# Kernel tuning notes

Measured on AMD Instinct MI355X. Metric: run time of the kernel, lower is better.

The kernel has to match this reference:

```python
import jax, jax.numpy as jnp
import numpy as np

NUM_CLASSES = 3
WINDOW = 5.0        # window_size for local connectivity
NUM_ITERS = 5       # mean-field iterations
THETA_BETA = 1.0    # smoothness kernel weight
TEMP = 1.0          # softmax temperature
H, W = 96, 96
B = 1


def setup_inputs() -> dict:
    key = jax.random.key(0)
    unary = jax.random.normal(key, (B, NUM_CLASSES, H, W), dtype=jnp.float32)
    # nn.Parameter(torch.eye(num_classes))
    compatibility = jnp.eye(NUM_CLASSES, dtype=jnp.float32)
    return {"unary": unary, "compatibility": compatibility}


def _pairwise_kernel(h, w):
    """Dense smoothness * local-connectivity kernel [N, N], N = h*w."""
    yy, xx = jnp.meshgrid(jnp.arange(h, dtype=jnp.float32),
                          jnp.arange(w, dtype=jnp.float32), indexing='ij')
    coords = jnp.stack([yy.ravel(), xx.ravel()], axis=-1)          # [N, 2]
    diff = coords[:, None, :] - coords[None, :, :]                 # [N, N, 2]
    dist = jnp.sqrt(jnp.sum(diff * diff, axis=-1))                 # cdist, [N, N]
    n = h * w
    conn = (dist <= WINDOW).astype(jnp.float32)
    conn = conn.at[jnp.arange(n), jnp.arange(n)].set(0.0)          # fill_diagonal_(0)
    smooth = jnp.exp(-THETA_BETA * dist)
    return smooth * conn                                           # [N, N]


def reference(unary, compatibility):
    b, c, h, w = unary.shape
    n = h * w
    unary_flat = unary.reshape(b, c, n)                            # [B, C, N]
    q = jax.nn.softmax(unary_flat / TEMP, axis=1)
    pairwise = _pairwise_kernel(h, w)                              # [N, N] (features=None path)
    for _ in range(NUM_ITERS):
        # messages[b,c,n] = sum_m pairwise[n,m] * q[b,c,m]  (bmm + transpose)
        messages = jnp.einsum('nm,bcm->bcn', pairwise, q)
        comp_msg = jnp.einsum('cd,bdn->bcn', compatibility, messages)
        q = jax.nn.softmax((unary_flat + comp_msg) / TEMP, axis=1)
    return q.reshape(b, c, h, w)
```

## Files before the change

kernel.cpp:

```cpp
#include <hip/hip_runtime.h>


constexpr int HH = 96, WW = 96, NN = HH * WW;
constexpr int T = 8, HALO = 5, EXT = T + 2 * HALO;

template <bool FIRST, bool LAST>
__global__ __launch_bounds__(64) void crf_iter(
    const float* __restrict__ unary,
    const float* __restrict__ comp,
    const float4* __restrict__ qin,
    float4* __restrict__ qnext,
    float* __restrict__ qout)
{
    __shared__ float4 qs[EXT][EXT + 1];
    __shared__ float wtab[121];

    const int tid = threadIdx.x;

    for (int i = tid; i < 121; i += 64) {
        int dy = i / 11 - 5, dx = i % 11 - 5;
        int d2 = dy * dy + dx * dx;
        wtab[i] = (d2 > 0 && d2 <= 25) ? expf(-sqrtf((float)d2)) : 0.0f;
    }

    const float c00 = comp[0], c01 = comp[1], c02 = comp[2];
    const float c10 = comp[3], c11 = comp[4], c12 = comp[5];
    const float c20 = comp[6], c21 = comp[7], c22 = comp[8];

    const int bx0 = blockIdx.x * T - HALO;
    const int by0 = blockIdx.y * T - HALO;

    for (int i = tid; i < EXT * EXT; i += 64) {
        int hy = i / EXT, hx = i - hy * EXT;
        int gy = by0 + hy, gx = bx0 + hx;
        float4 q = make_float4(0.f, 0.f, 0.f, 0.f);
        if (gy >= 0 && gy < HH && gx >= 0 && gx < WW) {
            int n = gy * WW + gx;
            if (FIRST) {
                float z0 = unary[n], z1 = unary[NN + n], z2 = unary[2 * NN + n];
                float mx = fmaxf(z0, fmaxf(z1, z2));
                float e0 = expf(z0 - mx), e1 = expf(z1 - mx), e2 = expf(z2 - mx);
                float inv = 1.0f / (e0 + e1 + e2);
                q = make_float4(e0 * inv, e1 * inv, e2 * inv, 0.f);
            } else {
                q = qin[n];
            }
        }
        qs[hy][hx] = q;
    }
    __syncthreads();

    const int ty = tid >> 3, tx = tid & 7;
    float m0 = 0.f, m1 = 0.f, m2 = 0.f;
    constexpr int XLO[11] = {5, 2, 1, 1, 1, 0, 1, 1, 1, 2, 5};
    constexpr int XHI[11] = {5, 8, 9, 9, 9, 10, 9, 9, 9, 8, 5};
#pragma unroll
    for (int dyi = 0; dyi < 11; ++dyi) {
#pragma unroll
        for (int dxi = XLO[dyi]; dxi <= XHI[dyi]; ++dxi) {
            float w = wtab[dyi * 11 + dxi];
            float4 q = qs[ty + dyi][tx + dxi];
            m0 = fmaf(w, q.x, m0);
            m1 = fmaf(w, q.y, m1);
            m2 = fmaf(w, q.z, m2);
        }
    }

    float t0 = c00 * m0 + c01 * m1 + c02 * m2;
    float t1 = c10 * m0 + c11 * m1 + c12 * m2;
    float t2 = c20 * m0 + c21 * m1 + c22 * m2;

    const int n = (blockIdx.y * T + ty) * WW + (blockIdx.x * T + tx);
    float z0 = unary[n] + t0;
    float z1 = unary[NN + n] + t1;
    float z2 = unary[2 * NN + n] + t2;

    float mx = fmaxf(z0, fmaxf(z1, z2));
    float e0 = expf(z0 - mx), e1 = expf(z1 - mx), e2 = expf(z2 - mx);
    float inv = 1.0f / (e0 + e1 + e2);

    if (LAST) {
        qout[n] = e0 * inv;
        qout[NN + n] = e1 * inv;
        qout[2 * NN + n] = e2 * inv;
    } else {
        qnext[n] = make_float4(e0 * inv, e1 * inv, e2 * inv, 0.f);
    }
}

extern "C" void kernel_launch(void* const* d_in, const int* in_sizes, int n_in,
                              void* d_out, int out_size, void* d_ws, size_t ws_size,
                              hipStream_t stream) {
    const float* unary = (const float*)d_in[0];
    const float* comp = (const float*)d_in[1];
    float* out = (float*)d_out;

    float4* qA = (float4*)d_ws;
    float4* qB = qA + NN;

    dim3 grid(WW / T, HH / T);
    dim3 block(64);

    crf_iter<true,  false><<<grid, block, 0, stream>>>(unary, comp, nullptr, qA, nullptr);
    crf_iter<false, false><<<grid, block, 0, stream>>>(unary, comp, qA, qB, nullptr);
    crf_iter<false, false><<<grid, block, 0, stream>>>(unary, comp, qB, qA, nullptr);
    crf_iter<false, false><<<grid, block, 0, stream>>>(unary, comp, qA, qB, nullptr);
    crf_iter<false, true ><<<grid, block, 0, stream>>>(unary, comp, qB, nullptr, out);
}
```

Measured before the change: 79.81 us.

## Fuse pairs of mean-field iterations into one kernel with doubled halo

Result: slower. 118.9 us (+48.9%).

```diff
diff --git a/kernel.cpp b/kernel.cpp
--- a/kernel.cpp
+++ b/kernel.cpp
@@ -2,7 +2,10 @@
 
 
 constexpr int HH = 96, WW = 96, NN = HH * WW;
-constexpr int T = 8, HALO = 5, EXT = T + 2 * HALO;
+constexpr int T = 8, HALO = 5;
+constexpr int EXT = T + 2 * HALO;
+constexpr int FEXT = T + 4 * HALO;
+constexpr int MEXT = T + 2 * HALO;
 
 template <bool FIRST, bool LAST>
 __global__ __launch_bounds__(64) void crf_iter(
@@ -88,6 +91,139 @@
     }
 }
 
+template <bool FIRST>
+__global__ __launch_bounds__(256) void crf_fused2(
+    const float* __restrict__ unary,
+    const float* __restrict__ comp,
+    const float4* __restrict__ qin,
+    float4* __restrict__ qnext)
+{
+    __shared__ float4 qs0[FEXT][FEXT + 1];
+    __shared__ float4 qs1[MEXT][MEXT + 1];
+    __shared__ float wtab[121];
+
+    const int tid = threadIdx.x;
+
+    if (tid < 121) {
+        int dy = tid / 11 - 5, dx = tid % 11 - 5;
+        int d2 = dy * dy + dx * dx;
+        wtab[tid] = (d2 > 0 && d2 <= 25) ? expf(-sqrtf((float)d2)) : 0.0f;
+    }
+
+    const float c00 = comp[0], c01 = comp[1], c02 = comp[2];
+    const float c10 = comp[3], c11 = comp[4], c12 = comp[5];
+    const float c20 = comp[6], c21 = comp[7], c22 = comp[8];
+
+    const int bx0 = blockIdx.x * T - 2 * HALO;
+    const int by0 = blockIdx.y * T - 2 * HALO;
+
+    for (int i = tid; i < FEXT * FEXT; i += 256) {
+        int sy = i / FEXT, sx = i - sy * FEXT;
+        int gy = by0 + sy, gx = bx0 + sx;
+        float4 q = make_float4(0.f, 0.f, 0.f, 0.f);
+        if (gy >= 0 && gy < HH && gx >= 0 && gx < WW) {
+            int n = gy * WW + gx;
+            if (FIRST) {
+                float z0 = unary[n], z1 = unary[NN + n], z2 = unary[2 * NN + n];
+                float mx = fmaxf(z0, fmaxf(z1, z2));
+                float e0 = expf(z0 - mx), e1 = expf(z1 - mx), e2 = expf(z2 - mx);
+                float inv = 1.0f / (e0 + e1 + e2);
+                q = make_float4(e0 * inv, e1 * inv, e2 * inv, 0.f);
+            } else {
+                q = qin[n];
+            }
+        }
+        qs0[sy][sx] = q;
+    }
+    __syncthreads();
+
+    if (tid < (MEXT / 2) * MEXT) {
+        const int iy = tid / MEXT;
+        const int ix = tid - iy * MEXT;
+        const int y1b = iy * 2, x1 = ix;
+
+        float m00 = 0.f, m01 = 0.f, m02 = 0.f;
+        float m10 = 0.f, m11 = 0.f, m12 = 0.f;
+
+        constexpr int DXLO2[12] = {5, 2, 1, 1, 1, 0, 0, 1, 1, 1, 2, 5};
+        constexpr int DXHI2[12] = {5, 8, 9, 9, 9, 10, 10, 9, 9, 9, 8, 5};
+#pragma unroll
+        for (int rr = 0; rr < 12; ++rr) {
+#pragma unroll
+            for (int dxi = DXLO2[rr]; dxi <= DXHI2[rr]; ++dxi) {
+                float4 q = qs0[y1b + rr][x1 + dxi];
+                if (rr <= 10) {
+                    float w = wtab[rr * 11 + dxi];
+                    m00 = fmaf(w, q.x, m00);
+                    m01 = fmaf(w, q.y, m01);
+                    m02 = fmaf(w, q.z, m02);
+                }
+                if (rr >= 1) {
+                    float w = wtab[(rr - 1) * 11 + dxi];
+                    m10 = fmaf(w, q.x, m10);
+                    m11 = fmaf(w, q.y, m11);
+                    m12 = fmaf(w, q.z, m12);
+                }
+            }
+        }
+
+#pragma unroll
+        for (int r = 0; r < 2; ++r) {
+            float M0 = r ? m10 : m00;
+            float M1 = r ? m11 : m01;
+            float M2 = r ? m12 : m02;
+            int y1 = y1b + r;
+            int gy = by0 + HALO + y1, gx = bx0 + HALO + x1;
+            float4 q1 = make_float4(0.f, 0.f, 0.f, 0.f);
+            if (gy >= 0 && gy < HH && gx >= 0 && gx < WW) {
+                int n = gy * WW + gx;
+                float t0 = c00 * M0 + c01 * M1 + c02 * M2;
+                float t1 = c10 * M0 + c11 * M1 + c12 * M2;
+                float t2 = c20 * M0 + c21 * M1 + c22 * M2;
+                float z0 = unary[n] + t0;
+                float z1 = unary[NN + n] + t1;
+                float z2 = unary[2 * NN + n] + t2;
+                float mx = fmaxf(z0, fmaxf(z1, z2));
+                float e0 = expf(z0 - mx), e1 = expf(z1 - mx), e2 = expf(z2 - mx);
+                float inv = 1.0f / (e0 + e1 + e2);
+                q1 = make_float4(e0 * inv, e1 * inv, e2 * inv, 0.f);
+            }
+            qs1[y1][x1] = q1;
+        }
+    }
+    __syncthreads();
+
+    if (tid < 64) {
+        const int ty = tid >> 3, tx = tid & 7;
+        float m0 = 0.f, m1 = 0.f, m2 = 0.f;
+        constexpr int XLO[11] = {5, 2, 1, 1, 1, 0, 1, 1, 1, 2, 5};
+        constexpr int XHI[11] = {5, 8, 9, 9, 9, 10, 9, 9, 9, 8, 5};
+#pragma unroll
+        for (int dyi = 0; dyi < 11; ++dyi) {
+#pragma unroll
+            for (int dxi = XLO[dyi]; dxi <= XHI[dyi]; ++dxi) {
+                float w = wtab[dyi * 11 + dxi];
+                float4 q = qs1[ty + dyi][tx + dxi];
+                m0 = fmaf(w, q.x, m0);
+                m1 = fmaf(w, q.y, m1);
+                m2 = fmaf(w, q.z, m2);
+            }
+        }
+        float t0 = c00 * m0 + c01 * m1 + c02 * m2;
+        float t1 = c10 * m0 + c11 * m1 + c12 * m2;
+        float t2 = c20 * m0 + c21 * m1 + c22 * m2;
+
+        const int n = (blockIdx.y * T + ty) * WW + (blockIdx.x * T + tx);
+        float z0 = unary[n] + t0;
+        float z1 = unary[NN + n] + t1;
+        float z2 = unary[2 * NN + n] + t2;
+        float mx = fmaxf(z0, fmaxf(z1, z2));
+        float e0 = expf(z0 - mx), e1 = expf(z1 - mx), e2 = expf(z2 - mx);
+        float inv = 1.0f / (e0 + e1 + e2);
+        qnext[n] = make_float4(e0 * inv, e1 * inv, e2 * inv, 0.f);
+    }
+}
+
 extern "C" void kernel_launch(void* const* d_in, const int* in_sizes, int n_in,
                               void* d_out, int out_size, void* d_ws, size_t ws_size,
                               hipStream_t stream) {
@@ -99,11 +235,8 @@
     float4* qB = qA + NN;
 
     dim3 grid(WW / T, HH / T);
-    dim3 block(64);
-
-    crf_iter<true,  false><<<grid, block, 0, stream>>>(unary, comp, nullptr, qA, nullptr);
-    crf_iter<false, false><<<grid, block, 0, stream>>>(unary, comp, qA, qB, nullptr);
-    crf_iter<false, false><<<grid, block, 0, stream>>>(unary, comp, qB, qA, nullptr);
-    crf_iter<false, false><<<grid, block, 0, stream>>>(unary, comp, qA, qB, nullptr);
-    crf_iter<false, true ><<<grid, block, 0, stream>>>(unary, comp, qB, nullptr, out);
+
+    crf_fused2<true ><<<grid, dim3(256), 0, stream>>>(unary, comp, nullptr, qA);
+    crf_fused2<false><<<grid, dim3(256), 0, stream>>>(unary, comp, qA, qB);
+    crf_iter<false, true><<<grid, dim3(64), 0, stream>>>(unary, comp, qB, nullptr, out);
 }
```
